# Optimization experiments

Hardware: AMD Instinct MI355X
Metric: run time of the kernel (lower is better)

Reference implementation:

```python
import jax, jax.numpy as jnp
import numpy as np

B, T, D, H = 4, 2048, 512, 8
K = D // H  # head dim = 64

def setup_inputs() -> dict:
    key = jax.random.key(0)
    k1, k2, k3, k4 = jax.random.split(key, 4)
    x = jax.random.normal(k1, (B, T, D), dtype=jnp.float32)
    # torch nn.Linear stores weight as [out_features, in_features]
    w_qkv = jax.random.normal(k2, (3 * D, D), dtype=jnp.float32) * (D ** -0.5)
    w_proj = jax.random.normal(k3, (D, D), dtype=jnp.float32) * (D ** -0.5)
    b_proj = jax.random.normal(k4, (D,), dtype=jnp.float32) * 0.01
    return {"x": x, "w_qkv": w_qkv, "w_proj": w_proj, "b_proj": b_proj}

def reference(x, w_qkv, w_proj, b_proj):
    Bx, Tx, Dx = x.shape
    # qkv projection (no bias): [B,T,3D]
    qkv = jnp.einsum('btd,ed->bte', x, w_qkv)
    q, k, v = jnp.split(qkv, 3, axis=-1)
    # [B,H,T,K]
    def heads(t):
        return t.reshape(Bx, Tx, H, K).transpose(0, 2, 1, 3)
    q, k, v = heads(q), heads(k), heads(v)
    # scaled scores with causal mask
    scores = jnp.einsum('bhqk,bhsk->bhqs', q, k) * (K ** -0.5)  # [B,H,T,T]
    causal = jnp.tril(jnp.ones((Tx, Tx), dtype=bool))
    scores = jnp.where(causal, scores, -jnp.inf)
    attn = jax.nn.softmax(scores, axis=-1)  # dropout p=0.0 -> identity
    out = jnp.einsum('bhqs,bhsk->bhqk', attn, v)  # [B,H,T,K]
    out = out.transpose(0, 2, 1, 3).reshape(Bx, Tx, Dx)
    out = jnp.einsum('btd,ed->bte', out, w_proj) + b_proj
    return out
```

## Files before the change

kernel.cpp:

```cpp
#include <hip/hip_runtime.h>
#include <hip/hip_bf16.h>


typedef unsigned short u16;
typedef __attribute__((ext_vector_type(8))) __bf16 bf16x8;
typedef __attribute__((ext_vector_type(8))) unsigned short u16x8;
typedef __attribute__((ext_vector_type(4))) unsigned short u16x4;
typedef __attribute__((ext_vector_type(4))) float f32x4;
typedef __attribute__((ext_vector_type(4))) unsigned u32x4;
typedef __attribute__((ext_vector_type(2))) unsigned u32x2;

#define DEV static __device__ __forceinline__

DEV void async16(const u16* g, u16* l) {
  __builtin_amdgcn_global_load_lds(
      (const __attribute__((address_space(1))) unsigned int*)g,
      (__attribute__((address_space(3))) unsigned int*)l, 16, 0, 0);
}
DEV u16x8 gld8(const u16* p) { return *(const u16x8*)p; }
DEV void lst8(u16* p, u16x8 v) { *(u16x8*)p = v; }
DEV bf16x8 ldsld8(const u16* p) {
  return __builtin_bit_cast(bf16x8, *(const u16x8*)p);
}
DEV f32x4 mfma16(bf16x8 a, bf16x8 b, f32x4 c) {
  return __builtin_amdgcn_mfma_f32_16x16x32_bf16(a, b, c, 0, 0, 0);
}
DEV u16 f2b(float f) {
  unsigned u = __builtin_bit_cast(unsigned, f);
  u += 0x7FFFu + ((u >> 16) & 1u);
  return (u16)(u >> 16);
}
DEV unsigned pk2(float x, float y) {
  __hip_bfloat162 t = __float22bfloat162_rn(float2{x, y});
  unsigned r;
  __builtin_memcpy(&r, &t, 4);
  return r;
}
DEV u16x8 pack8(f32x4 a, f32x4 b) {
  u32x4 t;
  t[0] = pk2(a[0], a[1]);
  t[1] = pk2(a[2], a[3]);
  t[2] = pk2(b[0], b[1]);
  t[3] = pk2(b[2], b[3]);
  return __builtin_bit_cast(u16x8, t);
}

__global__ void cvt_all(const float* __restrict__ x, const float* __restrict__ wq,
                        u16* __restrict__ xb, u16* __restrict__ wqb) {
  constexpr long NX = 8192L * 512 / 8;
  constexpr long NQ = 1536L * 512 / 8;
  const long i = (long)blockIdx.x * 256 + threadIdx.x;
  if (i < NX) {
    const float* p = x + i * 8;
    *(u16x8*)(xb + i * 8) = pack8(*(const f32x4*)p, *(const f32x4*)(p + 4));
  } else if (i < NX + NQ) {
    const long j = i - NX;
    const float* p = wq + j * 8;
    *(u16x8*)(wqb + j * 8) = pack8(*(const f32x4*)p, *(const f32x4*)(p + 4));
  }
}

__global__ void gemm_bb(const u16* __restrict__ A, const u16* __restrict__ Bt,
                        u16* __restrict__ qk, u16* __restrict__ vT, int K) {
  __shared__ __align__(16) u16 As[2][128 * 32];
  __shared__ __align__(16) u16 Bs[2][128 * 32];

  const int t = threadIdx.x, lane = t & 63, w = t >> 6;
  const int lane15 = lane & 15, quad = lane >> 4;
  const int wr = w >> 1, wc = w & 1;

  const int i = blockIdx.x;
  const int rt = (i & 7) | (((i >> 3) & 7) << 3);
  const int ct = i >> 6;
  const long row0 = (long)rt * 128;
  const int col0 = ct * 128;

  const int srow = w * 16 + (lane >> 2);
  const int scol = (lane & 3) * 8;
  const u16* Ag = A + (row0 + srow) * (long)K + scol;
  const u16* Bg = Bt + ((long)col0 + srow) * (long)K + scol;

  f32x4 acc[4][4];
#pragma unroll
  for (int ii = 0; ii < 4; ii++)
#pragma unroll
    for (int j = 0; j < 4; j++) acc[ii][j] = (f32x4)(0.0f);

  for (int k0 = 0; k0 < K; k0 += 64) {
    __syncthreads();
#pragma unroll
    for (int r = 0; r < 2; r++)
#pragma unroll
      for (int hf = 0; hf < 2; hf++) {
        async16(Ag + (long)r * 64 * K + k0 + hf * 32,
                &As[hf][(r * 64 + w * 16) * 32]);
        async16(Bg + (long)r * 64 * K + k0 + hf * 32,
                &Bs[hf][(r * 64 + w * 16) * 32]);
      }
    __syncthreads();

#pragma unroll
    for (int hf = 0; hf < 2; hf++) {
      bf16x8 a[4], b[4];
#pragma unroll
      for (int ii = 0; ii < 4; ii++)
        a[ii] = ldsld8(&As[hf][(wr * 64 + ii * 16 + lane15) * 32 + quad * 8]);
#pragma unroll
      for (int j = 0; j < 4; j++)
        b[j] = ldsld8(&Bs[hf][(wc * 64 + j * 16 + lane15) * 32 + quad * 8]);
#pragma unroll
      for (int ii = 0; ii < 4; ii++)
#pragma unroll
        for (int j = 0; j < 4; j++) acc[ii][j] = mfma16(a[ii], b[j], acc[ii][j]);
    }
  }

  if (col0 >= 1024) {
#pragma unroll
    for (int ii = 0; ii < 4; ii++)
#pragma unroll
      for (int j = 0; j < 4; j++) {
        const int hd = col0 - 1024 + wc * 64 + j * 16 + lane15;
        const long row = row0 + wr * 64 + ii * 16 + quad * 4;
        const long bb = row >> 11;
        const int s = (int)(row & 2047);
        u32x2 pr;
        pr[0] = pk2(acc[ii][j][0], acc[ii][j][1]);
        pr[1] = pk2(acc[ii][j][2], acc[ii][j][3]);
        *(u16x4*)(vT + (bb * 512 + hd) * 2048 + s) =
            __builtin_bit_cast(u16x4, pr);
      }
  } else {
#pragma unroll
    for (int ii = 0; ii < 4; ii++)
#pragma unroll
      for (int j = 0; j < 4; j++) {
        const int col = col0 + wc * 64 + j * 16 + lane15;
        const float sc = (col < 512) ? 0.18033688f : 1.0f;
#pragma unroll
        for (int r = 0; r < 4; r++) {
          const long row = row0 + wr * 64 + ii * 16 + quad * 4 + r;
          qk[row * 1024 + col] = f2b(acc[ii][j][r] * sc);
        }
      }
  }
}

__global__ void gemm_b64(const u16* __restrict__ A, const float* __restrict__ Bt,
                         const float* __restrict__ bias, float* __restrict__ C,
                         int N, int K) {
  __shared__ __align__(16) u16 As[2][128 * 32];
  __shared__ __align__(16) u16 Bs[2][64 * 32];

  const int t = threadIdx.x, lane = t & 63, w = t >> 6;
  const int lane15 = lane & 15, quad = lane >> 4;
  const int wr = w >> 1, wc = w & 1;

  const int i = blockIdx.x;
  const int rt = (i & 7) | (((i >> 3) & 7) << 3);
  const int ct = i >> 6;
  const long row0 = (long)rt * 128;
  const int col0 = ct * 64;

  const int srow = w * 16 + (lane >> 2);
  const int scol = (lane & 3) * 8;
  const u16* Ag = A + (row0 + srow) * (long)K + scol;

  const int brow = t >> 2, bc = (t & 3) * 16;
  const float* Bg = Bt + (long)(col0 + brow) * K + bc;
  u16* BsD = &Bs[bc >> 5][brow * 32 + (bc & 31)];

  f32x4 acc[4][2];
#pragma unroll
  for (int ii = 0; ii < 4; ii++)
#pragma unroll
    for (int j = 0; j < 2; j++) acc[ii][j] = (f32x4)(0.0f);

  f32x4 q0 = *(const f32x4*)Bg, q1 = *(const f32x4*)(Bg + 4);
  f32x4 q2 = *(const f32x4*)(Bg + 8), q3 = *(const f32x4*)(Bg + 12);

  for (int k0 = 0; k0 < K; k0 += 64) {
    __syncthreads();
#pragma unroll
    for (int r = 0; r < 2; r++)
#pragma unroll
      for (int hf = 0; hf < 2; hf++)
        async16(Ag + (long)r * 64 * K + k0 + hf * 32,
                &As[hf][(r * 64 + w * 16) * 32]);
    lst8(BsD, pack8(q0, q1));
    lst8(BsD + 8, pack8(q2, q3));
    __syncthreads();

    {
      const int kp = (k0 + 64 < K) ? k0 + 64 : k0;
      q0 = *(const f32x4*)(Bg + kp);     q1 = *(const f32x4*)(Bg + kp + 4);
      q2 = *(const f32x4*)(Bg + kp + 8); q3 = *(const f32x4*)(Bg + kp + 12);
    }

#pragma unroll
    for (int hf = 0; hf < 2; hf++) {
      bf16x8 a[4], b[2];
#pragma unroll
      for (int ii = 0; ii < 4; ii++)
        a[ii] = ldsld8(&As[hf][(wr * 64 + ii * 16 + lane15) * 32 + quad * 8]);
#pragma unroll
      for (int j = 0; j < 2; j++)
        b[j] = ldsld8(&Bs[hf][(wc * 32 + j * 16 + lane15) * 32 + quad * 8]);
#pragma unroll
      for (int ii = 0; ii < 4; ii++)
#pragma unroll
        for (int j = 0; j < 2; j++) acc[ii][j] = mfma16(a[ii], b[j], acc[ii][j]);
    }
  }

#pragma unroll
  for (int ii = 0; ii < 4; ii++)
#pragma unroll
    for (int j = 0; j < 2; j++) {
      const int col = col0 + wc * 32 + j * 16 + lane15;
      const float bv = bias[col];
#pragma unroll
      for (int r = 0; r < 4; r++) {
        const long row = row0 + wr * 64 + ii * 16 + quad * 4 + r;
        C[row * (long)N + col] = acc[ii][j][r] + bv;
      }
    }
}

__global__ void attn_v6(const u16* __restrict__ qk, const u16* __restrict__ vT,
                        u16* __restrict__ out) {
  constexpr int T = 2048, LDQ = 1024;
  __shared__ __align__(16) u16 Ks[64 * 72];
  __shared__ __align__(16) u16 Vs[64 * 72];
  __shared__ __align__(16) u16 Ps[4][16 * 72];

  const int t = threadIdx.x, lane = t & 63, w = t >> 6;
  const int lane15 = lane & 15, quad = lane >> 4;

  const int i = blockIdx.x;
  int qb = i & 31;
  if (i >= 512) qb = 31 - qb;
  const int h = (i >> 5) & 7;
  const int b = (i >> 8) & 3;
  const long baseq = (long)b * T * LDQ;
  const u16* vTb = vT + ((long)b * 512 + h * 64) * 2048;

  const u16* gq =
      qk + baseq + (long)(qb * 64 + w * 16 + lane15) * LDQ + h * 64 + quad * 8;
  const bf16x8 qa0 = __builtin_bit_cast(bf16x8, *(const u16x8*)gq);
  const bf16x8 qa1 = __builtin_bit_cast(bf16x8, *(const u16x8*)(gq + 32));

  const int srow = t >> 3, sc8 = (t & 7) * 8;

  const int nsb = qb + 1;

  u16x8 kr0, kr1, vr0, vr1;
  {
    const u16* gk = qk + baseq + (long)srow * LDQ + 512 + h * 64 + sc8;
    kr0 = gld8(gk); kr1 = gld8(gk + (long)32 * LDQ);
    const u16* gv = vTb + (long)srow * 2048 + sc8;
    vr0 = gld8(gv); vr1 = gld8(gv + (long)32 * 2048);
  }

  float lp[4] = {0.0f, 0.0f, 0.0f, 0.0f};
  f32x4 o[4];
#pragma unroll
  for (int j = 0; j < 4; j++) o[j] = (f32x4)(0.0f);

  const int qrow_base = qb * 64 + w * 16 + quad * 4;

  for (int sb = 0; sb < nsb; ++sb) {
    __syncthreads();
    lst8(&Ks[srow * 72 + sc8], kr0);
    lst8(&Ks[(srow + 32) * 72 + sc8], kr1);
    lst8(&Vs[srow * 72 + sc8], vr0);
    lst8(&Vs[(srow + 32) * 72 + sc8], vr1);
    __syncthreads();

    {
      const int sp = (sb + 1 < nsb) ? sb + 1 : sb;
      const u16* gk =
          qk + baseq + (long)(sp * 64 + srow) * LDQ + 512 + h * 64 + sc8;
      kr0 = gld8(gk); kr1 = gld8(gk + (long)32 * LDQ);
      const u16* gv = vTb + (long)srow * 2048 + sp * 64 + sc8;
      vr0 = gld8(gv); vr1 = gld8(gv + (long)32 * 2048);
    }

    f32x4 sf[4];
#pragma unroll
    for (int j = 0; j < 4; j++) {
      f32x4 z = (f32x4)(0.0f);
      z = mfma16(qa0, ldsld8(&Ks[(j * 16 + lane15) * 72 + quad * 8]), z);
      sf[j] = mfma16(qa1, ldsld8(&Ks[(j * 16 + lane15) * 72 + quad * 8 + 32]), z);
    }

    if (sb == qb) {
      const int scol_base = sb * 64 + lane15;
#pragma unroll
      for (int j = 0; j < 4; j++)
#pragma unroll
        for (int r = 0; r < 4; r++) {
          float p = exp2f(sf[j][r]);
          if (scol_base + j * 16 > qrow_base + r) p = 0.0f;
          sf[j][r] = p;
          lp[r] += p;
        }
    } else {
#pragma unroll
      for (int j = 0; j < 4; j++)
#pragma unroll
        for (int r = 0; r < 4; r++) {
          const float p = exp2f(sf[j][r]);
          sf[j][r] = p;
          lp[r] += p;
        }
    }

    u16* myP = Ps[w];
#pragma unroll
    for (int r = 0; r < 4; r++) {
      const int ro = (quad * 4 + r) * 72 + lane15;
      const unsigned v01 = pk2(sf[0][r], sf[1][r]);
      const unsigned v23 = pk2(sf[2][r], sf[3][r]);
      myP[ro] = (u16)v01;
      myP[ro + 16] = (u16)(v01 >> 16);
      myP[ro + 32] = (u16)v23;
      myP[ro + 48] = (u16)(v23 >> 16);
    }
    __asm__ __volatile__("" ::: "memory");
    const bf16x8 pa0 = ldsld8(&myP[lane15 * 72 + quad * 8]);
    const bf16x8 pa1 = ldsld8(&myP[lane15 * 72 + quad * 8 + 32]);
    __asm__ __volatile__("" ::: "memory");

#pragma unroll
    for (int j = 0; j < 4; j++) {
      const int d0 = (j * 16 + lane15) * 72;
      o[j] = mfma16(pa0, ldsld8(&Vs[d0 + quad * 8]), o[j]);
      o[j] = mfma16(pa1, ldsld8(&Vs[d0 + quad * 8 + 32]), o[j]);
    }
  }

#pragma unroll
  for (int off = 1; off < 16; off <<= 1)
#pragma unroll
    for (int r = 0; r < 4; r++) lp[r] += __shfl_xor(lp[r], off);

  const long orow0 = (long)b * T + qb * 64 + w * 16;
  float inv[4];
#pragma unroll
  for (int r = 0; r < 4; r++) inv[r] = 1.0f / lp[r];
#pragma unroll
  for (int j = 0; j < 4; j++)
#pragma unroll
    for (int r = 0; r < 4; r++)
      out[(orow0 + quad * 4 + r) * 512 + h * 64 + j * 16 + lane15] =
          f2b(o[j][r] * inv[r]);
}

extern "C" void kernel_launch(void* const* d_in, const int* in_sizes, int n_in,
                              void* d_out, int out_size, void* d_ws, size_t ws_size,
                              hipStream_t stream) {
  const float* x      = (const float*)d_in[0];
  const float* w_qkv  = (const float*)d_in[1];
  const float* w_proj = (const float*)d_in[2];
  const float* b_proj = (const float*)d_in[3];
  float* out = (float*)d_out;

  u16* qk = (u16*)d_ws;
  u16* vT = qk + (size_t)8192 * 1024;
  u16* xb = vT + (size_t)4 * 512 * 2048;
  u16* wqb = (u16*)d_out;

  cvt_all<<<2432, 256, 0, stream>>>(x, w_qkv, xb, wqb);
  gemm_bb<<<768, 256, 0, stream>>>(xb, wqb, qk, vT, 512);
  attn_v6<<<1024, 256, 0, stream>>>(qk, vT, xb);
  gemm_b64<<<512, 256, 0, stream>>>(xb, w_proj, b_proj, out, 512, 512);
}
```

Measured before the change: 153.5 us.

## Keep P in registers via transposed QK^T and permuted V layout, double-buffer K/V

The score MFMA now takes K as the A operand and Q as B, so each lane holds a column of scores. The V transpose in the QKV GEMM stores sequence indices permuted to match, so packed probabilities feed the PV MFMA directly from registers. This removes the per-wave LDS round-trip for P. K/V tiles are double-buffered in shared memory, which drops one barrier per iteration, and the row-sum reduction becomes two shuffles plus a broadcast. The cost is twice the K/V LDS footprint and a permuted V layout that is easy to get subtly wrong.

```diff
diff --git a/kernel.cpp b/kernel.cpp
--- a/kernel.cpp
+++ b/kernel.cpp
@@ -124,10 +124,11 @@
         const long row = row0 + wr * 64 + ii * 16 + quad * 4;
         const long bb = row >> 11;
         const int s = (int)(row & 2047);
+        const int ps = (s & ~31) | (((s >> 2) & 3) << 3) | (((s >> 4) & 1) << 2);
         u32x2 pr;
         pr[0] = pk2(acc[ii][j][0], acc[ii][j][1]);
         pr[1] = pk2(acc[ii][j][2], acc[ii][j][3]);
-        *(u16x4*)(vT + (bb * 512 + hd) * 2048 + s) =
+        *(u16x4*)(vT + (bb * 512 + hd) * 2048 + ps) =
             __builtin_bit_cast(u16x4, pr);
       }
   } else {
@@ -227,12 +228,11 @@
     }
 }
 
-__global__ void attn_v6(const u16* __restrict__ qk, const u16* __restrict__ vT,
+__global__ void attn_v7(const u16* __restrict__ qk, const u16* __restrict__ vT,
                         u16* __restrict__ out) {
   constexpr int T = 2048, LDQ = 1024;
-  __shared__ __align__(16) u16 Ks[64 * 72];
-  __shared__ __align__(16) u16 Vs[64 * 72];
-  __shared__ __align__(16) u16 Ps[4][16 * 72];
+  __shared__ __align__(16) u16 Ks[2][64 * 72];
+  __shared__ __align__(16) u16 Vs[2][64 * 72];
 
   const int t = threadIdx.x, lane = t & 63, w = t >> 6;
   const int lane15 = lane & 15, quad = lane >> 4;
@@ -251,7 +251,6 @@
   const bf16x8 qa1 = __builtin_bit_cast(bf16x8, *(const u16x8*)(gq + 32));
 
   const int srow = t >> 3, sc8 = (t & 7) * 8;
-
   const int nsb = qb + 1;
 
   u16x8 kr0, kr1, vr0, vr1;
@@ -261,24 +260,41 @@
     const u16* gv = vTb + (long)srow * 2048 + sc8;
     vr0 = gld8(gv); vr1 = gld8(gv + (long)32 * 2048);
   }
-
-  float lp[4] = {0.0f, 0.0f, 0.0f, 0.0f};
+  lst8(&Ks[0][srow * 72 + sc8], kr0);
+  lst8(&Ks[0][(srow + 32) * 72 + sc8], kr1);
+  lst8(&Vs[0][srow * 72 + sc8], vr0);
+  lst8(&Vs[0][(srow + 32) * 72 + sc8], vr1);
+  {
+    const int sp = (nsb > 1) ? 1 : 0;
+    const u16* gk =
+        qk + baseq + (long)(sp * 64 + srow) * LDQ + 512 + h * 64 + sc8;
+    kr0 = gld8(gk); kr1 = gld8(gk + (long)32 * LDQ);
+    const u16* gv = vTb + (long)srow * 2048 + sp * 64 + sc8;
+    vr0 = gld8(gv); vr1 = gld8(gv + (long)32 * 2048);
+  }
+
+  float lpl = 0.0f;
   f32x4 o[4];
 #pragma unroll
   for (int j = 0; j < 4; j++) o[j] = (f32x4)(0.0f);
 
-  const int qrow_base = qb * 64 + w * 16 + quad * 4;
+  const int qin = w * 16 + lane15;
 
   for (int sb = 0; sb < nsb; ++sb) {
-    __syncthreads();
-    lst8(&Ks[srow * 72 + sc8], kr0);
-    lst8(&Ks[(srow + 32) * 72 + sc8], kr1);
-    lst8(&Vs[srow * 72 + sc8], vr0);
-    lst8(&Vs[(srow + 32) * 72 + sc8], vr1);
-    __syncthreads();
+    const u16* Kc = Ks[sb & 1];
+    const u16* Vc = Vs[sb & 1];
+    u16* Kn = Ks[(sb + 1) & 1];
+    u16* Vn = Vs[(sb + 1) & 1];
+
+    __syncthreads();
+
+    lst8(&Kn[srow * 72 + sc8], kr0);
+    lst8(&Kn[(srow + 32) * 72 + sc8], kr1);
+    lst8(&Vn[srow * 72 + sc8], vr0);
+    lst8(&Vn[(srow + 32) * 72 + sc8], vr1);
 
     {
-      const int sp = (sb + 1 < nsb) ? sb + 1 : sb;
+      const int sp = (sb + 2 < nsb) ? sb + 2 : nsb - 1;
       const u16* gk =
           qk + baseq + (long)(sp * 64 + srow) * LDQ + 512 + h * 64 + sc8;
       kr0 = gld8(gk); kr1 = gld8(gk + (long)32 * LDQ);
@@ -290,20 +306,19 @@
 #pragma unroll
     for (int j = 0; j < 4; j++) {
       f32x4 z = (f32x4)(0.0f);
-      z = mfma16(qa0, ldsld8(&Ks[(j * 16 + lane15) * 72 + quad * 8]), z);
-      sf[j] = mfma16(qa1, ldsld8(&Ks[(j * 16 + lane15) * 72 + quad * 8 + 32]), z);
+      z = mfma16(ldsld8(&Kc[(j * 16 + lane15) * 72 + quad * 8]), qa0, z);
+      sf[j] = mfma16(ldsld8(&Kc[(j * 16 + lane15) * 72 + quad * 8 + 32]), qa1, z);
     }
 
     if (sb == qb) {
-      const int scol_base = sb * 64 + lane15;
 #pragma unroll
       for (int j = 0; j < 4; j++)
 #pragma unroll
         for (int r = 0; r < 4; r++) {
           float p = exp2f(sf[j][r]);
-          if (scol_base + j * 16 > qrow_base + r) p = 0.0f;
+          if (j * 16 + quad * 4 + r > qin) p = 0.0f;
           sf[j][r] = p;
-          lp[r] += p;
+          lpl += p;
         }
     } else {
 #pragma unroll
@@ -312,43 +327,33 @@
         for (int r = 0; r < 4; r++) {
           const float p = exp2f(sf[j][r]);
           sf[j][r] = p;
-          lp[r] += p;
+          lpl += p;
         }
     }
 
-    u16* myP = Ps[w];
-#pragma unroll
-    for (int r = 0; r < 4; r++) {
-      const int ro = (quad * 4 + r) * 72 + lane15;
-      const unsigned v01 = pk2(sf[0][r], sf[1][r]);
-      const unsigned v23 = pk2(sf[2][r], sf[3][r]);
-      myP[ro] = (u16)v01;
-      myP[ro + 16] = (u16)(v01 >> 16);
-      myP[ro + 32] = (u16)v23;
-      myP[ro + 48] = (u16)(v23 >> 16);
-    }
-    __asm__ __volatile__("" ::: "memory");
-    const bf16x8 pa0 = ldsld8(&myP[lane15 * 72 + quad * 8]);
-    const bf16x8 pa1 = ldsld8(&myP[lane15 * 72 + quad * 8 + 32]);
-    __asm__ __volatile__("" ::: "memory");
+    u32x4 pw0, pw1;
+    pw0[0] = pk2(sf[0][0], sf[0][1]); pw0[1] = pk2(sf[0][2], sf[0][3]);
+    pw0[2] = pk2(sf[1][0], sf[1][1]); pw0[3] = pk2(sf[1][2], sf[1][3]);
+    pw1[0] = pk2(sf[2][0], sf[2][1]); pw1[1] = pk2(sf[2][2], sf[2][3]);
+    pw1[2] = pk2(sf[3][0], sf[3][1]); pw1[3] = pk2(sf[3][2], sf[3][3]);
+    const bf16x8 pa0 = __builtin_bit_cast(bf16x8, pw0);
+    const bf16x8 pa1 = __builtin_bit_cast(bf16x8, pw1);
 
 #pragma unroll
     for (int j = 0; j < 4; j++) {
       const int d0 = (j * 16 + lane15) * 72;
-      o[j] = mfma16(pa0, ldsld8(&Vs[d0 + quad * 8]), o[j]);
-      o[j] = mfma16(pa1, ldsld8(&Vs[d0 + quad * 8 + 32]), o[j]);
-    }
-  }
-
-#pragma unroll
-  for (int off = 1; off < 16; off <<= 1)
-#pragma unroll
-    for (int r = 0; r < 4; r++) lp[r] += __shfl_xor(lp[r], off);
+      o[j] = mfma16(pa0, ldsld8(&Vc[d0 + quad * 8]), o[j]);
+      o[j] = mfma16(pa1, ldsld8(&Vc[d0 + quad * 8 + 32]), o[j]);
+    }
+  }
+
+  lpl += __shfl_xor(lpl, 16);
+  lpl += __shfl_xor(lpl, 32);
 
   const long orow0 = (long)b * T + qb * 64 + w * 16;
   float inv[4];
 #pragma unroll
-  for (int r = 0; r < 4; r++) inv[r] = 1.0f / lp[r];
+  for (int r = 0; r < 4; r++) inv[r] = 1.0f / __shfl(lpl, quad * 4 + r);
 #pragma unroll
   for (int j = 0; j < 4; j++)
 #pragma unroll
@@ -373,6 +378,6 @@
 
   cvt_all<<<2432, 256, 0, stream>>>(x, w_qkv, xb, wqb);
   gemm_bb<<<768, 256, 0, stream>>>(xb, wqb, qk, vT, 512);
-  attn_v6<<<1024, 256, 0, stream>>>(qk, vT, xb);
+  attn_v7<<<1024, 256, 0, stream>>>(qk, vT, xb);
   gemm_b64<<<512, 256, 0, stream>>>(xb, w_proj, b_proj, out, 512, 512);
 }
```

Measured after the change: 150.1 us. 1.02x faster.
